# Optimization experiments

Hardware: AMD Instinct MI355X
Metric: run time of the kernel (lower is better)

Reference implementation:

```python
import jax, jax.numpy as jnp
import numpy as np

L, B, E, H, G = 4, 8, 1024, 16, 4096
N_IMG, T_TXT, V = 256, 64, 16385
EPS = 1e-6

def _ln(x, b, s=None):
    m = jnp.mean(x, axis=-1, keepdims=True)
    v = jnp.var(x, axis=-1, keepdims=True)
    y = (x - m) * jax.lax.rsqrt(v + EPS)
    if s is not None:
        y = y * s
    return y + b

def _attend(keys, values, queries, mask, w_out):
    # keys/values: [B,Tk,E]; queries: [B,Tq,E]; mask: [B,Tk]
    Bq, Tq, Eq = queries.shape
    d = Eq // H
    k = keys.reshape(keys.shape[0], -1, H, d)
    v = values.reshape(values.shape[0], -1, H, d)
    q = queries.reshape(Bq, Tq, H, d) / jnp.asarray(np.sqrt(d), queries.dtype)
    bias = jnp.where(mask, 0.0, -jnp.inf)
    w = jnp.einsum('bqhd,bkhd->bhqk', q, k) + bias[:, None, None, :]
    w = jax.nn.softmax(w, axis=-1)
    o = jnp.einsum('bhqk,bkhd->bqhd', w, v).reshape(Bq, Tq, Eq)
    return o @ w_out

def setup_inputs() -> dict:
    key = jax.random.key(0)
    ks = jax.random.split(key, 24)
    sc = 0.02
    nrm = lambda i, shape: sc * jax.random.normal(ks[i], shape, jnp.float32)
    return {
        "encoder_state": jax.random.normal(ks[0], (B, T_TXT, E), jnp.float32),
        "attention_state": 0.5 * jax.random.normal(ks[1], (L, 2 * B, N_IMG, E), jnp.float32),
        "attention_mask": jnp.ones((B, T_TXT), jnp.bool_),
        "prev_token": 16384,
        "token_index": 100,
        "embed_tok": nrm(2, (V, E)),
        "embed_pos": nrm(3, (N_IMG, E)),
        "lnemb_s": jnp.ones((E,), jnp.float32),
        "lnemb_b": jnp.zeros((E,), jnp.float32),
        "pre_self_ln_b": jnp.zeros((L, E), jnp.float32),
        "self_q": nrm(4, (L, E, E)),
        "self_k": nrm(5, (L, E, E)),
        "self_v": nrm(6, (L, E, E)),
        "self_o": nrm(7, (L, E, E)),
        "self_ln_s": jnp.ones((L, E), jnp.float32),
        "self_ln_b": jnp.zeros((L, E), jnp.float32),
        "pre_enc_ln_b": jnp.zeros((L, E), jnp.float32),
        "enc_q": nrm(8, (L, E, E)),
        "enc_k": nrm(9, (L, E, E)),
        "enc_v": nrm(10, (L, E, E)),
        "enc_o": nrm(11, (L, E, E)),
        "enc_ln_s": jnp.ones((L, E), jnp.float32),
        "enc_ln_b": jnp.zeros((L, E), jnp.float32),
        "glu_ln0_b": jnp.zeros((L, E), jnp.float32),
        "glu_fc0": nrm(12, (L, E, G)),
        "glu_fc1": nrm(13, (L, E, G)),
        "glu_ln1_b": jnp.zeros((L, G), jnp.float32),
        "glu_fc2": nrm(14, (L, G, E)),
        "final_ln_b": jnp.zeros((E,), jnp.float32),
        "lm_head_w": nrm(15, (E, V)),
    }

def reference(encoder_state, attention_state, attention_mask, prev_token, token_index, embed_tok, embed_pos, lnemb_s, lnemb_b, pre_self_ln_b, self_q, self_k, self_v, self_o, self_ln_s, self_ln_b, pre_enc_ln_b, enc_q, enc_k, enc_v, enc_o, enc_ln_s, enc_ln_b, glu_ln0_b, glu_fc0, glu_fc1, glu_ln1_b, glu_fc2, final_ln_b, lm_head_w):
    ones = jnp.ones((B, 1), jnp.int32)
    x = embed_tok[prev_token * ones] + embed_pos[token_index * ones]  # [B,1,E]
    x = _ln(x, lnemb_b, lnemb_s)
    self_mask = jnp.tile(jnp.arange(N_IMG) < token_index + 1, (B, 1))  # [B,N_IMG]

    def step(x, xs):
        (psb, sq, sk, sv, so, sls, slb, peb, eq, ek, ev, eo, els, elb,
         g0b, gf0, gf1, g1b, gf2, ast) = xs
        res = x
        h = _ln(x, psb)
        k, v, q = h @ sk, h @ sv, h @ sq
        ast = jax.lax.dynamic_update_slice(ast, jnp.concatenate([k, v]).astype(jnp.float32), (0, token_index, 0))
        h = _attend(ast[:B], ast[B:], q, self_mask, so).astype(x.dtype)
        x = res + _ln(h, slb, sls)
        res = x
        h = _ln(x, peb)
        h = _attend(encoder_state @ ek, encoder_state @ ev, h @ eq, attention_mask, eo)
        x = res + _ln(h, elb, els)
        res = x
        h = _ln(x, g0b)
        h = _ln(jax.nn.gelu(h @ gf0, approximate=False) * (h @ gf1), g1b)
        x = res + h @ gf2
        return x, ast

    xs = (pre_self_ln_b, self_q, self_k, self_v, self_o, self_ln_s, self_ln_b,
          pre_enc_ln_b, enc_q, enc_k, enc_v, enc_o, enc_ln_s, enc_ln_b,
          glu_ln0_b, glu_fc0, glu_fc1, glu_ln1_b, glu_fc2, attention_state)
    x, attention_state = jax.lax.scan(step, x, xs)
    x = _ln(x, final_ln_b)
    logits = x @ lm_head_w  # [B,1,V]
    return logits, attention_state
```

## Files before the change

### kernel.cpp

```cpp
#include <hip/hip_runtime.h>
#include <math.h>

#define EPSF 1e-6f

#define NL 4
#define NB 8
#define NE 1024
#define NH 16
#define NG 4096
#define NIMG 256
#define NTT 64
#define NV 16385
#define NVPAD 17408

#define P_QKV   0
#define P_FC01  786432
#define P_FC2   1835008
#define P_LM    2359296
#define SSPART  4587520
#define SEPART  4718592
#define XBUF    4849664
#define DH1     4857856
#define DX2     4866048
#define DX3     4874240
#define DH3     4882432
#define DHG     4890624
#define DHF     4923392
#define MFLAG   4931584

__device__ inline void wave_red2(float& a, float& b) {
#pragma unroll
  for (int o = 32; o; o >>= 1) { a += __shfl_xor(a, o); b += __shfl_xor(b, o); }
}

__device__ inline void block_red2(float& s, float& ss, float* tmp) {
  wave_red2(s, ss);
  int wv = threadIdx.x >> 6, ln = threadIdx.x & 63;
  if (ln == 0) { tmp[wv] = s; tmp[4 + wv] = ss; }
  __syncthreads();
  s = tmp[0] + tmp[1] + tmp[2] + tmp[3];
  ss = tmp[4] + tmp[5] + tmp[6] + tmp[7];
  __syncthreads();
}

__device__ inline float4 f4add(float4 a, float4 b) {
  return make_float4(a.x + b.x, a.y + b.y, a.z + b.z, a.w + b.w);
}

struct MvPartP {
  const float* W0; const float* W1; const float* W2;
  float* pout;
  const float* hsrc;
  int K, N, NPAD, CB, KS;
};

__global__ __launch_bounds__(256) void mv_part(MvPartP p) {
  __shared__ float h[8 * 64];
  const int tid = threadIdx.x;
  const int per = p.CB * p.KS;
  const int m = blockIdx.x / per, rem = blockIdx.x % per;
  const int ks = rem / p.CB, cb = rem % p.CB;
  const int BK = p.K / p.KS;
  const int k0 = ks * BK;
  const int n0 = cb * 1024;
  const int bk4 = BK >> 2;
  for (int i = tid; i < 8 * bk4; i += 256) {
    int r = i / bk4, q = i - r * bk4;
    reinterpret_cast<float4*>(h)[i] =
        *reinterpret_cast<const float4*>(p.hsrc + (size_t)r * p.K + k0 + q * 4);
  }
  __syncthreads();

  const int nb = n0 + tid * 4;
  if (nb >= p.N) return;
  const float* W = (m == 0) ? p.W0 : (m == 1) ? p.W1 : p.W2;
  float* pr = p.pout + (size_t)(m * p.KS + ks) * 8 * p.NPAD;
  const float* wp = W + (size_t)k0 * p.N + nb;

  if (nb + 3 < p.N) {
    float4 acc[8];
#pragma unroll
    for (int r = 0; r < 8; ++r) acc[r] = make_float4(0.f, 0.f, 0.f, 0.f);
    for (int kk = 0; kk < BK; kk += 8) {
      float4 w[8];
#pragma unroll
      for (int j = 0; j < 8; ++j)
        w[j] = *reinterpret_cast<const float4*>(wp + (size_t)(kk + j) * p.N);
#pragma unroll
      for (int j = 0; j < 8; ++j) {
#pragma unroll
        for (int r = 0; r < 8; ++r) {
          float hv = h[r * BK + kk + j];
          acc[r].x += hv * w[j].x; acc[r].y += hv * w[j].y;
          acc[r].z += hv * w[j].z; acc[r].w += hv * w[j].w;
        }
      }
    }
#pragma unroll
    for (int r = 0; r < 8; ++r)
      *reinterpret_cast<float4*>(pr + (size_t)r * p.NPAD + nb) = acc[r];
  } else {
    for (int c = 0; c < 4; ++c) {
      if (nb + c >= p.N) break;
      float acc[8] = {0.f, 0.f, 0.f, 0.f, 0.f, 0.f, 0.f, 0.f};
      for (int kk = 0; kk < BK; ++kk) {
        float w = wp[(size_t)kk * p.N + c];
#pragma unroll
        for (int r = 0; r < 8; ++r) acc[r] += h[r * BK + kk] * w;
      }
#pragma unroll
      for (int r = 0; r < 8; ++r) pr[(size_t)r * p.NPAD + nb + c] = acc[r];
    }
  }
}

__global__ __launch_bounds__(256) void embed_copy(const float* __restrict__ tok,
    const float* __restrict__ pos, const int* __restrict__ prev, const int* __restrict__ tixp,
    const float* __restrict__ lnb, const float* __restrict__ lns,
    const float* __restrict__ psb0, const void* __restrict__ maskp,
    float* __restrict__ x0, float* __restrict__ h1, unsigned* __restrict__ mflag,
    const float4* __restrict__ astv, float4* __restrict__ oastv) {
  __shared__ float tmp[8];
  int bid = blockIdx.x, tid = threadIdx.x;
  if (bid < 8) {
    int b = bid;
    const float* te = tok + (size_t)prev[0] * NE;
    const float* pe = pos + (size_t)tixp[0] * NE;
    float4 t4 = *reinterpret_cast<const float4*>(te + tid * 4);
    float4 p4 = *reinterpret_cast<const float4*>(pe + tid * 4);
    float4 v = make_float4(t4.x + p4.x, t4.y + p4.y, t4.z + p4.z, t4.w + p4.w);
    float s = v.x + v.y + v.z + v.w;
    float ss = v.x * v.x + v.y * v.y + v.z * v.z + v.w * v.w;
    block_red2(s, ss, tmp);
    float m = s / NE, rs = rsqrtf(ss / NE - m * m + EPSF);
    float4 sc = *reinterpret_cast<const float4*>(lns + tid * 4);
    float4 bi = *reinterpret_cast<const float4*>(lnb + tid * 4);
    float4 x;
    x.x = (v.x - m) * rs * sc.x + bi.x; x.y = (v.y - m) * rs * sc.y + bi.y;
    x.z = (v.z - m) * rs * sc.z + bi.z; x.w = (v.w - m) * rs * sc.w + bi.w;
    *reinterpret_cast<float4*>(x0 + (size_t)b * NE + tid * 4) = x;
    float s2 = x.x + x.y + x.z + x.w;
    float ss2 = x.x * x.x + x.y * x.y + x.z * x.z + x.w * x.w;
    block_red2(s2, ss2, tmp);
    float m2 = s2 / NE, rs2 = rsqrtf(ss2 / NE - m2 * m2 + EPSF);
    float4 b2 = *reinterpret_cast<const float4*>(psb0 + tid * 4);
    float4 o;
    o.x = (x.x - m2) * rs2 + b2.x; o.y = (x.y - m2) * rs2 + b2.y;
    o.z = (x.z - m2) * rs2 + b2.z; o.w = (x.w - m2) * rs2 + b2.w;
    *reinterpret_cast<float4*>(h1 + (size_t)b * NE + tid * 4) = o;
    return;
  }
  if (bid == 8) {
    __shared__ int f;
    if (tid == 0) f = 1;
    __syncthreads();
    if (tid < 128) { if (((const unsigned*)maskp)[tid] > 1u) f = 0; }
    __syncthreads();
    if (tid == 0) *mflag = f ? 1u : 2u;
  }
  const int n4 = NL * 16 * NIMG * (NE / 4);
  for (int i = (bid - 8) * 256 + tid; i < n4; i += 4096 * 256) oastv[i] = astv[i];
}

__global__ __launch_bounds__(256) void ln_fc2(const float* __restrict__ P,
    const float* __restrict__ resid, const float* __restrict__ bias,
    float* __restrict__ xout, float* __restrict__ hout, int KS) {
  __shared__ float tmp[8];
  int b = blockIdx.x, tid = threadIdx.x;
  int col = tid * 4;
  float4 acc = *reinterpret_cast<const float4*>(resid + (size_t)b * NE + col);
  const float* base = P + (size_t)b * 1024 + col;
  for (int ks = 0; ks < KS; ks += 8) {
    float4 w[8];
#pragma unroll
    for (int j = 0; j < 8; ++j)
      w[j] = *reinterpret_cast<const float4*>(base + (size_t)(ks + j) * 8192);
#pragma unroll
    for (int j = 0; j < 8; ++j) acc = f4add(acc, w[j]);
  }
  *reinterpret_cast<float4*>(xout + (size_t)b * NE + col) = acc;
  float s = acc.x + acc.y + acc.z + acc.w;
  float ss = acc.x * acc.x + acc.y * acc.y + acc.z * acc.z + acc.w * acc.w;
  block_red2(s, ss, tmp);
  float m = s / NE, rs = rsqrtf(ss / NE - m * m + EPSF);
  float4 bi = *reinterpret_cast<const float4*>(bias + col);
  float4 o;
  o.x = (acc.x - m) * rs + bi.x; o.y = (acc.y - m) * rs + bi.y;
  o.z = (acc.z - m) * rs + bi.z; o.w = (acc.w - m) * rs + bi.w;
  *reinterpret_cast<float4*>(hout + (size_t)b * NE + col) = o;
}

__global__ __launch_bounds__(256) void ln_res_sum(const float* __restrict__ xres,
    const float* __restrict__ part, const float* __restrict__ lns1,
    const float* __restrict__ lnb1, const float* __restrict__ lnb2,
    float* __restrict__ xstore, float* __restrict__ hout) {
  __shared__ float tmp[8];
  int b = blockIdx.x, tid = threadIdx.x;
  int col = tid * 4;
  float4 sv = make_float4(0.f, 0.f, 0.f, 0.f);
  const float* base = part + (size_t)b * 1024 + col;
#pragma unroll
  for (int h = 0; h < 16; h += 8) {
    float4 w[8];
#pragma unroll
    for (int j = 0; j < 8; ++j)
      w[j] = *reinterpret_cast<const float4*>(base + (size_t)(h + j) * 8192);
#pragma unroll
    for (int j = 0; j < 8; ++j) sv = f4add(sv, w[j]);
  }
  float s = sv.x + sv.y + sv.z + sv.w;
  float ss = sv.x * sv.x + sv.y * sv.y + sv.z * sv.z + sv.w * sv.w;
  block_red2(s, ss, tmp);
  float m1 = s / NE, rs1 = rsqrtf(ss / NE - m1 * m1 + EPSF);
  float4 xv = *reinterpret_cast<const float4*>(xres + (size_t)b * NE + col);
  float4 sc1 = *reinterpret_cast<const float4*>(lns1 + col);
  float4 b1 = *reinterpret_cast<const float4*>(lnb1 + col);
  float4 v;
  v.x = xv.x + (sv.x - m1) * rs1 * sc1.x + b1.x;
  v.y = xv.y + (sv.y - m1) * rs1 * sc1.y + b1.y;
  v.z = xv.z + (sv.z - m1) * rs1 * sc1.z + b1.z;
  v.w = xv.w + (sv.w - m1) * rs1 * sc1.w + b1.w;
  *reinterpret_cast<float4*>(xstore + (size_t)b * NE + col) = v;
  float s2 = v.x + v.y + v.z + v.w;
  float ss2 = v.x * v.x + v.y * v.y + v.z * v.z + v.w * v.w;
  block_red2(s2, ss2, tmp);
  float m2 = s2 / NE, rs2 = rsqrtf(ss2 / NE - m2 * m2 + EPSF);
  float4 b2 = *reinterpret_cast<const float4*>(lnb2 + col);
  float4 o;
  o.x = (v.x - m2) * rs2 + b2.x; o.y = (v.y - m2) * rs2 + b2.y;
  o.z = (v.z - m2) * rs2 + b2.z; o.w = (v.w - m2) * rs2 + b2.w;
  *reinterpret_cast<float4*>(hout + (size_t)b * NE + col) = o;
}

__global__ __launch_bounds__(256) void gelu_ln_sum(const float* __restrict__ P,
    const float* __restrict__ lnb, float* __restrict__ hout) {
  __shared__ float tmp[8];
  int b = blockIdx.x, tid = threadIdx.x;
  float4 g[4];
  float s = 0.f, ss = 0.f;
#pragma unroll
  for (int q = 0; q < 4; ++q) {
    int col = (tid + 256 * q) * 4;
    float4 a = make_float4(0.f, 0.f, 0.f, 0.f);
    float4 bb = make_float4(0.f, 0.f, 0.f, 0.f);
    const float* baseA = P + (size_t)b * 4096 + col;
    const float* baseB = P + ((size_t)16 * 8 + b) * 4096 + col;
#pragma unroll
    for (int ks = 0; ks < 16; ++ks) {
      a = f4add(a, *reinterpret_cast<const float4*>(baseA + (size_t)ks * 32768));
      bb = f4add(bb, *reinterpret_cast<const float4*>(baseB + (size_t)ks * 32768));
    }
    float4 gg;
    gg.x = 0.5f * a.x * (1.f + erff(a.x * 0.70710678118f)) * bb.x;
    gg.y = 0.5f * a.y * (1.f + erff(a.y * 0.70710678118f)) * bb.y;
    gg.z = 0.5f * a.z * (1.f + erff(a.z * 0.70710678118f)) * bb.z;
    gg.w = 0.5f * a.w * (1.f + erff(a.w * 0.70710678118f)) * bb.w;
    g[q] = gg;
    s += gg.x + gg.y + gg.z + gg.w;
    ss += gg.x * gg.x + gg.y * gg.y + gg.z * gg.z + gg.w * gg.w;
  }
  block_red2(s, ss, tmp);
  float m = s / NG, rs = rsqrtf(ss / NG - m * m + EPSF);
#pragma unroll
  for (int q = 0; q < 4; ++q) {
    int col = (tid + 256 * q) * 4;
    float4 bi = *reinterpret_cast<const float4*>(lnb + col);
    float4 o;
    o.x = (g[q].x - m) * rs + bi.x; o.y = (g[q].y - m) * rs + bi.y;
    o.z = (g[q].z - m) * rs + bi.z; o.w = (g[q].w - m) * rs + bi.w;
    *reinterpret_cast<float4*>(hout + (size_t)b * NG + col) = o;
  }
}

__global__ __launch_bounds__(256) void attn_fused(const float* __restrict__ Pqkv,
    const float* __restrict__ ast_l, const int* __restrict__ tixp,
    const float* __restrict__ Wso, float* __restrict__ spart, float* __restrict__ oast_l) {
  int b = blockIdx.x >> 4, hh = blockIdx.x & 15;
  int tid = threadIdx.x;
  int tix0 = tixp[0];
  int tixc = tix0 < 0 ? 0 : (tix0 > 255 ? 255 : tix0);
  int T = tixc + 1;
  __shared__ float qv[64];
  __shared__ float kf[64];
  __shared__ float vf[64];
  __shared__ float scb[256];
  __shared__ float red[256];
  __shared__ float pv[1024];
  __shared__ float ov[64];
  if (tid < 192) {
    int m = tid >> 6, d = tid & 63;
    const float* bp = Pqkv + (size_t)(m * 32) * 8192 + (size_t)b * 1024 + hh * 64 + d;
    float acc = 0.f;
#pragma unroll
    for (int ks = 0; ks < 32; ++ks) acc += bp[(size_t)ks * 8192];
    if (m == 2) qv[d] = acc * 0.125f;
    else {
      if (m == 0) kf[d] = acc; else vf[d] = acc;
      if (tix0 >= 0 && tix0 < NIMG) {
        int row = (m == 0) ? b : 8 + b;
        oast_l[((size_t)row * NIMG + tix0) * NE + hh * 64 + d] = acc;
      }
    }
  }
  __syncthreads();
  float sj = -INFINITY;
  if (tid < T) {
    const float* kr = (tid == tixc) ? kf : (ast_l + ((size_t)b * NIMG + tid) * NE + hh * 64);
    float s = 0.f;
#pragma unroll
    for (int d0 = 0; d0 < 64; d0 += 4) {
      float4 k4 = *reinterpret_cast<const float4*>(kr + d0);
      s += qv[d0] * k4.x + qv[d0 + 1] * k4.y + qv[d0 + 2] * k4.z + qv[d0 + 3] * k4.w;
    }
    sj = s;
  }
  red[tid] = sj; __syncthreads();
  for (int o = 128; o; o >>= 1) { if (tid < o) red[tid] = fmaxf(red[tid], red[tid + o]); __syncthreads(); }
  float mx = red[0]; __syncthreads();
  float e = (tid < T) ? __expf(sj - mx) : 0.f;
  red[tid] = e; __syncthreads();
  for (int o = 128; o; o >>= 1) { if (tid < o) red[tid] += red[tid + o]; __syncthreads(); }
  float inv = 1.f / red[0];
  scb[tid] = e * inv;
  __syncthreads();
  {
    int c = tid >> 4, d4 = (tid & 15) * 4;
    float4 a = make_float4(0.f, 0.f, 0.f, 0.f);
    for (int j = c; j < T; j += 16) {
      const float* vr = (j == tixc) ? vf : (ast_l + ((size_t)(8 + b) * NIMG + j) * NE + hh * 64);
      float4 v4 = *reinterpret_cast<const float4*>(vr + d4);
      float w = scb[j];
      a.x += w * v4.x; a.y += w * v4.y; a.z += w * v4.z; a.w += w * v4.w;
    }
    pv[c * 64 + d4 + 0] = a.x; pv[c * 64 + d4 + 1] = a.y;
    pv[c * 64 + d4 + 2] = a.z; pv[c * 64 + d4 + 3] = a.w;
  }
  __syncthreads();
  if (tid < 64) {
    float s = 0.f;
#pragma unroll
    for (int c = 0; c < 16; ++c) s += pv[c * 64 + tid];
    ov[tid] = s;
  }
  __syncthreads();
  {
    int nb = tid * 4;
    const float* wp = Wso + (size_t)(hh * 64) * NE + nb;
    float4 acc = make_float4(0.f, 0.f, 0.f, 0.f);
    for (int d = 0; d < 64; d += 8) {
      float4 w[8];
#pragma unroll
      for (int j = 0; j < 8; ++j)
        w[j] = *reinterpret_cast<const float4*>(wp + (size_t)(d + j) * NE);
#pragma unroll
      for (int j = 0; j < 8; ++j) {
        float o = ov[d + j];
        acc.x += o * w[j].x; acc.y += o * w[j].y; acc.z += o * w[j].z; acc.w += o * w[j].w;
      }
    }
    *reinterpret_cast<float4*>(spart + ((size_t)hh * 8 + b) * 1024 + nb) = acc;
  }
}

__global__ __launch_bounds__(256) void cross_fused(const float* __restrict__ xres,
    const float* __restrict__ sspart, const float* __restrict__ sls,
    const float* __restrict__ slb, const float* __restrict__ peb,
    const float* __restrict__ Weq, const float* __restrict__ Wek,
    const float* __restrict__ Wev, const float* __restrict__ Weo,
    const float* __restrict__ X, const void* __restrict__ maskp,
    const unsigned* __restrict__ mflag, float* __restrict__ x2store,
    float* __restrict__ spart) {
  int b = blockIdx.x >> 4, hh = blockIdx.x & 15;
  int tid = threadIdx.x;
  __shared__ float vecA[NE];
  __shared__ float vecB[NE];
  __shared__ float red[256];
  __shared__ float w_[NTT];
  __shared__ float qv[64];
  __shared__ float oe[64];
  __shared__ float tmp[8];
  int mi32 = (*mflag == 1u);
  {
    int col = tid * 4;
    float4 sv = make_float4(0.f, 0.f, 0.f, 0.f);
    const float* base = sspart + (size_t)b * 1024 + col;
#pragma unroll
    for (int h = 0; h < 16; h += 8) {
      float4 w[8];
#pragma unroll
      for (int j = 0; j < 8; ++j)
        w[j] = *reinterpret_cast<const float4*>(base + (size_t)(h + j) * 8192);
#pragma unroll
      for (int j = 0; j < 8; ++j) sv = f4add(sv, w[j]);
    }
    float s = sv.x + sv.y + sv.z + sv.w;
    float ss = sv.x * sv.x + sv.y * sv.y + sv.z * sv.z + sv.w * sv.w;
    block_red2(s, ss, tmp);
    float m1 = s / NE, rs1 = rsqrtf(ss / NE - m1 * m1 + EPSF);
    float4 xv = *reinterpret_cast<const float4*>(xres + (size_t)b * NE + col);
    float4 sc1 = *reinterpret_cast<const float4*>(sls + col);
    float4 b1 = *reinterpret_cast<const float4*>(slb + col);
    float4 v;
    v.x = xv.x + (sv.x - m1) * rs1 * sc1.x + b1.x;
    v.y = xv.y + (sv.y - m1) * rs1 * sc1.y + b1.y;
    v.z = xv.z + (sv.z - m1) * rs1 * sc1.z + b1.z;
    v.w = xv.w + (sv.w - m1) * rs1 * sc1.w + b1.w;
    if (hh == 0)
      *reinterpret_cast<float4*>(x2store + (size_t)b * NE + col) = v;
    float s2 = v.x + v.y + v.z + v.w;
    float ss2 = v.x * v.x + v.y * v.y + v.z * v.z + v.w * v.w;
    block_red2(s2, ss2, tmp);
    float m2 = s2 / NE, rs2 = rsqrtf(ss2 / NE - m2 * m2 + EPSF);
    float4 b2 = *reinterpret_cast<const float4*>(peb + col);
    float4 o;
    o.x = (v.x - m2) * rs2 + b2.x; o.y = (v.y - m2) * rs2 + b2.y;
    o.z = (v.z - m2) * rs2 + b2.z; o.w = (v.w - m2) * rs2 + b2.w;
    reinterpret_cast<float4*>(vecA)[tid] = o;
  }
  __syncthreads();

  {
    int d4 = (tid & 15) * 4, ech = tid >> 4;
    const float* base = Weq + hh * 64 + d4;
    float4 a = make_float4(0.f, 0.f, 0.f, 0.f);
    for (int e = ech * 64; e < ech * 64 + 64; e += 8) {
      float4 w[8];
#pragma unroll
      for (int j = 0; j < 8; ++j)
        w[j] = *reinterpret_cast<const float4*>(base + (size_t)(e + j) * NE);
#pragma unroll
      for (int j = 0; j < 8; ++j) {
        float hv = vecA[e + j];
        a.x += hv * w[j].x; a.y += hv * w[j].y; a.z += hv * w[j].z; a.w += hv * w[j].w;
      }
    }
    vecB[ech * 64 + d4 + 0] = a.x; vecB[ech * 64 + d4 + 1] = a.y;
    vecB[ech * 64 + d4 + 2] = a.z; vecB[ech * 64 + d4 + 3] = a.w;
  }
  __syncthreads();
  if (tid < 64) {
    float s = 0.f;
#pragma unroll
    for (int c = 0; c < 16; ++c) s += vecB[c * 64 + tid];
    qv[tid] = s;
  }
  __syncthreads();

  {
    float qwtmp[4];
#pragma unroll
    for (int jj = 0; jj < 4; ++jj) {
      int e = tid + 256 * jj;
      const float* wr = Wek + (size_t)e * NE + hh * 64;
      float a = 0.f;
#pragma unroll
      for (int d0 = 0; d0 < 64; d0 += 4) {
        float4 w4 = *reinterpret_cast<const float4*>(wr + d0);
        a += qv[d0] * w4.x + qv[d0 + 1] * w4.y + qv[d0 + 2] * w4.z + qv[d0 + 3] * w4.w;
      }
      qwtmp[jj] = a;
    }
#pragma unroll
    for (int jj = 0; jj < 4; ++jj) vecB[tid + 256 * jj] = qwtmp[jj];
  }
  __syncthreads();

  {
    int t = tid & 63, ec = tid >> 6;
    const float* xr = X + ((size_t)b * NTT + t) * NE + ec * 256;
    float part = 0.f;
#pragma unroll 4
    for (int i = 0; i < 256; i += 4) {
      float4 x4 = *reinterpret_cast<const float4*>(xr + i);
      part += vecB[ec * 256 + i] * x4.x + vecB[ec * 256 + i + 1] * x4.y +
              vecB[ec * 256 + i + 2] * x4.z + vecB[ec * 256 + i + 3] * x4.w;
    }
    red[ec * 64 + t] = part;
  }
  __syncthreads();
  float sco = -INFINITY;
  if (tid < 64) {
    float s = (red[tid] + red[64 + tid] + red[128 + tid] + red[192 + tid]) * 0.125f;
    int idx = b * NTT + tid;
    bool valid = mi32 ? (((const int*)maskp)[idx] != 0)
                      : (((const unsigned char*)maskp)[idx] != 0);
    sco = valid ? s : -INFINITY;
  }
  __syncthreads();
  red[tid] = (tid < 64) ? sco : -INFINITY; __syncthreads();
  for (int o = 128; o; o >>= 1) { if (tid < o) red[tid] = fmaxf(red[tid], red[tid + o]); __syncthreads(); }
  float mx = red[0]; __syncthreads();
  float e = (tid < 64) ? __expf(sco - mx) : 0.f;
  red[tid] = e; __syncthreads();
  for (int o = 128; o; o >>= 1) { if (tid < o) red[tid] += red[tid + o]; __syncthreads(); }
  if (tid < 64) w_[tid] = e / red[0];
  __syncthreads();

  {
    float4 a = make_float4(0.f, 0.f, 0.f, 0.f);
    const float* xb = X + (size_t)b * NTT * NE + tid * 4;
    for (int t = 0; t < NTT; t += 4) {
#pragma unroll
      for (int j = 0; j < 4; ++j) {
        float4 x4 = *reinterpret_cast<const float4*>(xb + (size_t)(t + j) * NE);
        float w = w_[t + j];
        a.x += w * x4.x; a.y += w * x4.y; a.z += w * x4.z; a.w += w * x4.w;
      }
    }
    reinterpret_cast<float4*>(vecA)[tid] = a;
  }
  __syncthreads();

  {
    int d4 = (tid & 15) * 4, ech = tid >> 4;
    const float* base = Wev + hh * 64 + d4;
    float4 a = make_float4(0.f, 0.f, 0.f, 0.f);
    for (int e = ech * 64; e < ech * 64 + 64; e += 8) {
      float4 w[8];
#pragma unroll
      for (int j = 0; j < 8; ++j)
        w[j] = *reinterpret_cast<const float4*>(base + (size_t)(e + j) * NE);
#pragma unroll
      for (int j = 0; j < 8; ++j) {
        float hv = vecA[e + j];
        a.x += hv * w[j].x; a.y += hv * w[j].y; a.z += hv * w[j].z; a.w += hv * w[j].w;
      }
    }
    vecB[ech * 64 + d4 + 0] = a.x; vecB[ech * 64 + d4 + 1] = a.y;
    vecB[ech * 64 + d4 + 2] = a.z; vecB[ech * 64 + d4 + 3] = a.w;
  }
  __syncthreads();
  if (tid < 64) {
    float s = 0.f;
#pragma unroll
    for (int c = 0; c < 16; ++c) s += vecB[c * 64 + tid];
    oe[tid] = s;
  }
  __syncthreads();

  {
    int nb = tid * 4;
    const float* wp = Weo + (size_t)(hh * 64) * NE + nb;
    float4 acc = make_float4(0.f, 0.f, 0.f, 0.f);
    for (int d = 0; d < 64; d += 8) {
      float4 w[8];
#pragma unroll
      for (int j = 0; j < 8; ++j)
        w[j] = *reinterpret_cast<const float4*>(wp + (size_t)(d + j) * NE);
#pragma unroll
      for (int j = 0; j < 8; ++j) {
        float o = oe[d + j];
        acc.x += o * w[j].x; acc.y += o * w[j].y; acc.z += o * w[j].z; acc.w += o * w[j].w;
      }
    }
    *reinterpret_cast<float4*>(spart + ((size_t)hh * 8 + b) * 1024 + nb) = acc;
  }
}

__global__ __launch_bounds__(256) void reduce_logits(const float* __restrict__ P,
                                                     float* __restrict__ logits) {
  int r = blockIdx.x / 17, cc = blockIdx.x % 17;
  int col = cc * 1024 + threadIdx.x * 4;
  if (col >= NV) return;
  if (col + 3 < NV) {
    const float* base = P + (size_t)r * NVPAD + col;
    float4 acc = make_float4(0.f, 0.f, 0.f, 0.f);
    for (int ks = 0; ks < 16; ks += 8) {
      float4 w[8];
#pragma unroll
      for (int j = 0; j < 8; ++j)
        w[j] = *reinterpret_cast<const float4*>(base + (size_t)(ks + j) * 8 * NVPAD);
#pragma unroll
      for (int j = 0; j < 8; ++j) acc = f4add(acc, w[j]);
    }
    *reinterpret_cast<float4*>(logits + (size_t)r * NV + col) = acc;
  } else {
    for (int c = 0; c < 4 && col + c < NV; ++c) {
      float a = 0.f;
      for (int ks = 0; ks < 16; ++ks) a += P[((size_t)ks * 8 + r) * NVPAD + col + c];
      logits[(size_t)r * NV + col + c] = a;
    }
  }
}

extern "C" void kernel_launch(void* const* d_in, const int* in_sizes, int n_in,
                              void* d_out, int out_size, void* d_ws, size_t ws_size,
                              hipStream_t stream) {
  const float* enc_state = (const float*)d_in[0];
  const float* ast_in    = (const float*)d_in[1];
  const void* amask      = d_in[2];
  const int* prev = (const int*)d_in[3];
  const int* tix  = (const int*)d_in[4];
  const float* embed_tok = (const float*)d_in[5];
  const float* embed_pos = (const float*)d_in[6];
  const float* lnemb_s = (const float*)d_in[7];
  const float* lnemb_b = (const float*)d_in[8];
  const float* psb = (const float*)d_in[9];
  const float* Wsq = (const float*)d_in[10];
  const float* Wsk = (const float*)d_in[11];
  const float* Wsv = (const float*)d_in[12];
  const float* Wso = (const float*)d_in[13];
  const float* sls = (const float*)d_in[14];
  const float* slb = (const float*)d_in[15];
  const float* peb = (const float*)d_in[16];
  const float* Weq = (const float*)d_in[17];
  const float* Wek = (const float*)d_in[18];
  const float* Wev = (const float*)d_in[19];
  const float* Weo = (const float*)d_in[20];
  const float* els = (const float*)d_in[21];
  const float* elb = (const float*)d_in[22];
  const float* g0b = (const float*)d_in[23];
  const float* Wf0 = (const float*)d_in[24];
  const float* Wf1 = (const float*)d_in[25];
  const float* g1b = (const float*)d_in[26];
  const float* Wf2 = (const float*)d_in[27];
  const float* flb = (const float*)d_in[28];
  const float* Wlm = (const float*)d_in[29];

  float* ws = (float*)d_ws;
  float* logits = (float*)d_out;
  float* out_ast = logits + (size_t)NB * NV;

  embed_copy<<<4104, 256, 0, stream>>>(embed_tok, embed_pos, prev, tix, lnemb_b, lnemb_s,
                                       psb, amask, ws + XBUF, ws + DH1,
                                       (unsigned*)(ws + MFLAG),
                                       (const float4*)ast_in, (float4*)out_ast);

  for (int l = 0; l < NL; ++l) {
    size_t wE = (size_t)l * NE * NE;
    size_t wG = (size_t)l * NE * NG;

    if (l > 0) {
      ln_fc2<<<NB, 256, 0, stream>>>(ws + P_FC2, ws + DX3, psb + (size_t)l * NE,
                                     ws + XBUF, ws + DH1, 64);
    }
    {
      MvPartP p{}; p.W0 = Wsk + wE; p.W1 = Wsv + wE; p.W2 = Wsq + wE;
      p.pout = ws + P_QKV; p.hsrc = ws + DH1;
      p.K = NE; p.N = NE; p.NPAD = NE; p.CB = 1; p.KS = 32;
      mv_part<<<3 * 32, 256, 0, stream>>>(p);
    }
    attn_fused<<<NB * NH, 256, 0, stream>>>(ws + P_QKV,
                                            ast_in + (size_t)l * 16 * NIMG * NE, tix,
                                            Wso + wE, ws + SSPART,
                                            out_ast + (size_t)l * 16 * NIMG * NE);
    cross_fused<<<NB * NH, 256, 0, stream>>>(ws + XBUF, ws + SSPART,
                                             sls + (size_t)l * NE, slb + (size_t)l * NE,
                                             peb + (size_t)l * NE,
                                             Weq + wE, Wek + wE, Wev + wE, Weo + wE,
                                             enc_state, amask,
                                             (const unsigned*)(ws + MFLAG),
                                             ws + DX2, ws + SEPART);
    ln_res_sum<<<NB, 256, 0, stream>>>(ws + DX2, ws + SEPART, els + (size_t)l * NE,
                                       elb + (size_t)l * NE, g0b + (size_t)l * NE,
                                       ws + DX3, ws + DH3);
    {
      MvPartP p{}; p.W0 = Wf0 + wG; p.W1 = Wf1 + wG;
      p.pout = ws + P_FC01; p.hsrc = ws + DH3;
      p.K = NE; p.N = NG; p.NPAD = NG; p.CB = 4; p.KS = 16;
      mv_part<<<2 * 4 * 16, 256, 0, stream>>>(p);
    }
    gelu_ln_sum<<<NB, 256, 0, stream>>>(ws + P_FC01, g1b + (size_t)l * NG, ws + DHG);
    {
      MvPartP p{}; p.W0 = Wf2 + (size_t)l * NG * NE;
      p.pout = ws + P_FC2; p.hsrc = ws + DHG;
      p.K = NG; p.N = NE; p.NPAD = NE; p.CB = 1; p.KS = 64;
      mv_part<<<64, 256, 0, stream>>>(p);
    }
  }
  ln_fc2<<<NB, 256, 0, stream>>>(ws + P_FC2, ws + DX3, flb, ws + XBUF, ws + DHF, 64);
  {
    MvPartP p{}; p.W0 = Wlm;
    p.pout = ws + P_LM; p.hsrc = ws + DHF;
    p.K = NE; p.N = NV; p.NPAD = NVPAD; p.CB = 17; p.KS = 16;
    mv_part<<<17 * 16, 256, 0, stream>>>(p);
  }
  reduce_logits<<<NB * 17, 256, 0, stream>>>(ws + P_LM, logits);
}
```

Before: 570.5 us.

## Fuse LayerNorm into matvec input staging and rebalance split-K partitioning

Partial sums of the residual and GELU outputs are now reduced by wider-grid combine kernels that also emit per-chunk mean/variance statistics. The following matvec kernel applies the LayerNorm while staging its input into shared memory, which removes the separate 8-block ln_fc2 and gelu_ln_sum kernels. The QKV, FC0/1 and FC2 matvecs also switch to a one-column-per-thread variant with more column blocks and fewer K splits, which shrinks the partial buffers and spreads the reduction work across more blocks. In exchange, every block recomputes the statistics, and scalar weight loads replace float4 loads.

```diff
diff --git a/kernel.cpp b/kernel.cpp
--- a/kernel.cpp
+++ b/kernel.cpp
@@ -14,19 +14,19 @@
 #define NVPAD 17408
 
 #define P_QKV   0
-#define P_FC01  786432
-#define P_FC2   1835008
-#define P_LM    2359296
-#define SSPART  4587520
-#define SEPART  4718592
-#define XBUF    4849664
-#define DH1     4857856
-#define DX2     4866048
-#define DX3     4874240
-#define DH3     4882432
-#define DHG     4890624
-#define DHF     4923392
-#define MFLAG   4931584
+#define P_FC01  393216
+#define P_FC2   917504
+#define P_LM    1179648
+#define SSPART  3407872
+#define SEPART  3538944
+#define XBUF    3670016
+#define DX2     3678208
+#define DX3     3686400
+#define DH3     3694592
+#define DG      3702784
+#define XSTAT   3735552
+#define GSTAT   3735616
+#define MFLAG   3735744
 
 __device__ inline void wave_red2(float& a, float& b) {
 #pragma unroll
@@ -47,79 +47,172 @@
   return make_float4(a.x + b.x, a.y + b.y, a.z + b.z, a.w + b.w);
 }
 
-struct MvPartP {
+struct MvP {
   const float* W0; const float* W1; const float* W2;
   float* pout;
   const float* hsrc;
-  int K, N, NPAD, CB, KS;
+  const float* xsrc;
+  const float* stats;
+  const float* bias;
+  int K, N, NPAD, CB, KS, mode, nchunk;
 };
 
-__global__ __launch_bounds__(256) void mv_part(MvPartP p) {
-  __shared__ float h[8 * 64];
+template <int C>
+__global__ __launch_bounds__(256) void mv_k(MvP p) {
+  __shared__ float h[8 * 128];
+  __shared__ float mrs[8][2];
   const int tid = threadIdx.x;
   const int per = p.CB * p.KS;
   const int m = blockIdx.x / per, rem = blockIdx.x % per;
   const int ks = rem / p.CB, cb = rem % p.CB;
   const int BK = p.K / p.KS;
   const int k0 = ks * BK;
-  const int n0 = cb * 1024;
+  const int n0 = cb * 256 * C;
   const int bk4 = BK >> 2;
-  for (int i = tid; i < 8 * bk4; i += 256) {
-    int r = i / bk4, q = i - r * bk4;
-    reinterpret_cast<float4*>(h)[i] =
-        *reinterpret_cast<const float4*>(p.hsrc + (size_t)r * p.K + k0 + q * 4);
-  }
-  __syncthreads();
-
-  const int nb = n0 + tid * 4;
-  if (nb >= p.N) return;
+
+  if (p.mode == 1) {
+    if (tid < 8) {
+      float s = 0.f, ss = 0.f;
+      for (int c = 0; c < p.nchunk; ++c) {
+        s += p.stats[(tid * p.nchunk + c) * 2];
+        ss += p.stats[(tid * p.nchunk + c) * 2 + 1];
+      }
+      float mean = s / p.K;
+      mrs[tid][0] = mean;
+      mrs[tid][1] = rsqrtf(ss / p.K - mean * mean + EPSF);
+    }
+    __syncthreads();
+    for (int i = tid; i < 8 * bk4; i += 256) {
+      int r = i / bk4, q = i - r * bk4;
+      float4 xv = *reinterpret_cast<const float4*>(p.xsrc + (size_t)r * p.K + k0 + q * 4);
+      float4 bi = *reinterpret_cast<const float4*>(p.bias + k0 + q * 4);
+      float mm = mrs[r][0], rs = mrs[r][1];
+      float4 o = make_float4((xv.x - mm) * rs + bi.x, (xv.y - mm) * rs + bi.y,
+                             (xv.z - mm) * rs + bi.z, (xv.w - mm) * rs + bi.w);
+      *reinterpret_cast<float4*>(h + r * BK + q * 4) = o;
+    }
+  } else {
+    for (int i = tid; i < 8 * bk4; i += 256) {
+      int r = i / bk4, q = i - r * bk4;
+      *reinterpret_cast<float4*>(h + r * BK + q * 4) =
+          *reinterpret_cast<const float4*>(p.hsrc + (size_t)r * p.K + k0 + q * 4);
+    }
+  }
+  __syncthreads();
+
   const float* W = (m == 0) ? p.W0 : (m == 1) ? p.W1 : p.W2;
   float* pr = p.pout + (size_t)(m * p.KS + ks) * 8 * p.NPAD;
-  const float* wp = W + (size_t)k0 * p.N + nb;
-
-  if (nb + 3 < p.N) {
-    float4 acc[8];
-#pragma unroll
-    for (int r = 0; r < 8; ++r) acc[r] = make_float4(0.f, 0.f, 0.f, 0.f);
+
+  if (C == 1) {
+    int col = n0 + tid;
+    if (col >= p.N) return;
+    const float* wp = W + (size_t)k0 * p.N + col;
+    float acc[8] = {0.f, 0.f, 0.f, 0.f, 0.f, 0.f, 0.f, 0.f};
     for (int kk = 0; kk < BK; kk += 8) {
-      float4 w[8];
-#pragma unroll
-      for (int j = 0; j < 8; ++j)
-        w[j] = *reinterpret_cast<const float4*>(wp + (size_t)(kk + j) * p.N);
+      float w[8];
+#pragma unroll
+      for (int j = 0; j < 8; ++j) w[j] = wp[(size_t)(kk + j) * p.N];
 #pragma unroll
       for (int j = 0; j < 8; ++j) {
 #pragma unroll
-        for (int r = 0; r < 8; ++r) {
-          float hv = h[r * BK + kk + j];
-          acc[r].x += hv * w[j].x; acc[r].y += hv * w[j].y;
-          acc[r].z += hv * w[j].z; acc[r].w += hv * w[j].w;
+        for (int r = 0; r < 8; ++r) acc[r] += h[r * BK + kk + j] * w[j];
+      }
+    }
+#pragma unroll
+    for (int r = 0; r < 8; ++r) pr[(size_t)r * p.NPAD + col] = acc[r];
+  } else {
+    int nb = n0 + tid * 4;
+    if (nb >= p.N) return;
+    const float* wp = W + (size_t)k0 * p.N + nb;
+    if (nb + 3 < p.N) {
+      float4 acc[8];
+#pragma unroll
+      for (int r = 0; r < 8; ++r) acc[r] = make_float4(0.f, 0.f, 0.f, 0.f);
+      for (int kk = 0; kk < BK; kk += 8) {
+        float4 w[8];
+#pragma unroll
+        for (int j = 0; j < 8; ++j)
+          w[j] = *reinterpret_cast<const float4*>(wp + (size_t)(kk + j) * p.N);
+#pragma unroll
+        for (int j = 0; j < 8; ++j) {
+#pragma unroll
+          for (int r = 0; r < 8; ++r) {
+            float hv = h[r * BK + kk + j];
+            acc[r].x += hv * w[j].x; acc[r].y += hv * w[j].y;
+            acc[r].z += hv * w[j].z; acc[r].w += hv * w[j].w;
+          }
         }
       }
-    }
-#pragma unroll
-    for (int r = 0; r < 8; ++r)
-      *reinterpret_cast<float4*>(pr + (size_t)r * p.NPAD + nb) = acc[r];
-  } else {
-    for (int c = 0; c < 4; ++c) {
-      if (nb + c >= p.N) break;
-      float acc[8] = {0.f, 0.f, 0.f, 0.f, 0.f, 0.f, 0.f, 0.f};
-      for (int kk = 0; kk < BK; ++kk) {
-        float w = wp[(size_t)kk * p.N + c];
-#pragma unroll
-        for (int r = 0; r < 8; ++r) acc[r] += h[r * BK + kk] * w;
-      }
-#pragma unroll
-      for (int r = 0; r < 8; ++r) pr[(size_t)r * p.NPAD + nb + c] = acc[r];
-    }
+#pragma unroll
+      for (int r = 0; r < 8; ++r)
+        *reinterpret_cast<float4*>(pr + (size_t)r * p.NPAD + nb) = acc[r];
+    } else {
+      for (int c = 0; c < 4; ++c) {
+        if (nb + c >= p.N) break;
+        float acc[8] = {0.f, 0.f, 0.f, 0.f, 0.f, 0.f, 0.f, 0.f};
+        for (int kk = 0; kk < BK; ++kk) {
+          float w = wp[(size_t)kk * p.N + c];
+#pragma unroll
+          for (int r = 0; r < 8; ++r) acc[r] += h[r * BK + kk] * w;
+        }
+#pragma unroll
+        for (int r = 0; r < 8; ++r) pr[(size_t)r * p.NPAD + nb + c] = acc[r];
+      }
+    }
+  }
+}
+
+__global__ __launch_bounds__(256) void combine_g(const float* __restrict__ P,
+    float* __restrict__ g, float* __restrict__ gstats) {
+  __shared__ float tmp[8];
+  int b = blockIdx.x >> 3, ch = blockIdx.x & 7;
+  int tid = threadIdx.x;
+  int col = ch * 512 + tid * 2;
+  const float* baseA = P + (size_t)b * NG + col;
+  const float* baseB = P + ((size_t)8 * 8 + b) * NG + col;
+  float2 a = make_float2(0.f, 0.f), bb = make_float2(0.f, 0.f);
+#pragma unroll
+  for (int ks = 0; ks < 8; ++ks) {
+    float2 pa = *reinterpret_cast<const float2*>(baseA + (size_t)ks * 8 * NG);
+    float2 pb = *reinterpret_cast<const float2*>(baseB + (size_t)ks * 8 * NG);
+    a.x += pa.x; a.y += pa.y; bb.x += pb.x; bb.y += pb.y;
+  }
+  float2 gg;
+  gg.x = 0.5f * a.x * (1.f + erff(a.x * 0.70710678118f)) * bb.x;
+  gg.y = 0.5f * a.y * (1.f + erff(a.y * 0.70710678118f)) * bb.y;
+  *reinterpret_cast<float2*>(g + (size_t)b * NG + col) = gg;
+  float s = gg.x + gg.y, ss = gg.x * gg.x + gg.y * gg.y;
+  block_red2(s, ss, tmp);
+  if (tid == 0) {
+    gstats[(b * 8 + ch) * 2] = s;
+    gstats[(b * 8 + ch) * 2 + 1] = ss;
+  }
+}
+
+__global__ __launch_bounds__(256) void combine_x(const float* __restrict__ P,
+    const float* __restrict__ resid, float* __restrict__ xout, float* __restrict__ xstats) {
+  __shared__ float tmp[8];
+  int b = blockIdx.x >> 2, ch = blockIdx.x & 3;
+  int tid = threadIdx.x;
+  int col = ch * 256 + tid;
+  float acc = resid[(size_t)b * NE + col];
+  const float* base = P + (size_t)b * NE + col;
+#pragma unroll
+  for (int ks = 0; ks < 32; ++ks) acc += base[(size_t)ks * 8 * NE];
+  xout[(size_t)b * NE + col] = acc;
+  float s = acc, ss = acc * acc;
+  block_red2(s, ss, tmp);
+  if (tid == 0) {
+    xstats[(b * 4 + ch) * 2] = s;
+    xstats[(b * 4 + ch) * 2 + 1] = ss;
   }
 }
 
 __global__ __launch_bounds__(256) void embed_copy(const float* __restrict__ tok,
     const float* __restrict__ pos, const int* __restrict__ prev, const int* __restrict__ tixp,
     const float* __restrict__ lnb, const float* __restrict__ lns,
-    const float* __restrict__ psb0, const void* __restrict__ maskp,
-    float* __restrict__ x0, float* __restrict__ h1, unsigned* __restrict__ mflag,
-    const float4* __restrict__ astv, float4* __restrict__ oastv) {
+    const void* __restrict__ maskp, float* __restrict__ x0, float* __restrict__ xstats,
+    unsigned* __restrict__ mflag, const float4* __restrict__ astv, float4* __restrict__ oastv) {
   __shared__ float tmp[8];
   int bid = blockIdx.x, tid = threadIdx.x;
   if (bid < 8) {
@@ -142,12 +235,11 @@
     float s2 = x.x + x.y + x.z + x.w;
     float ss2 = x.x * x.x + x.y * x.y + x.z * x.z + x.w * x.w;
     block_red2(s2, ss2, tmp);
-    float m2 = s2 / NE, rs2 = rsqrtf(ss2 / NE - m2 * m2 + EPSF);
-    float4 b2 = *reinterpret_cast<const float4*>(psb0 + tid * 4);
-    float4 o;
-    o.x = (x.x - m2) * rs2 + b2.x; o.y = (x.y - m2) * rs2 + b2.y;
-    o.z = (x.z - m2) * rs2 + b2.z; o.w = (x.w - m2) * rs2 + b2.w;
-    *reinterpret_cast<float4*>(h1 + (size_t)b * NE + tid * 4) = o;
+    if (tid == 0) {
+      xstats[(b * 4 + 0) * 2] = s2; xstats[(b * 4 + 0) * 2 + 1] = ss2;
+#pragma unroll
+      for (int c = 1; c < 4; ++c) { xstats[(b * 4 + c) * 2] = 0.f; xstats[(b * 4 + c) * 2 + 1] = 0.f; }
+    }
     return;
   }
   if (bid == 8) {
@@ -160,34 +252,6 @@
   }
   const int n4 = NL * 16 * NIMG * (NE / 4);
   for (int i = (bid - 8) * 256 + tid; i < n4; i += 4096 * 256) oastv[i] = astv[i];
-}
-
-__global__ __launch_bounds__(256) void ln_fc2(const float* __restrict__ P,
-    const float* __restrict__ resid, const float* __restrict__ bias,
-    float* __restrict__ xout, float* __restrict__ hout, int KS) {
-  __shared__ float tmp[8];
-  int b = blockIdx.x, tid = threadIdx.x;
-  int col = tid * 4;
-  float4 acc = *reinterpret_cast<const float4*>(resid + (size_t)b * NE + col);
-  const float* base = P + (size_t)b * 1024 + col;
-  for (int ks = 0; ks < KS; ks += 8) {
-    float4 w[8];
-#pragma unroll
-    for (int j = 0; j < 8; ++j)
-      w[j] = *reinterpret_cast<const float4*>(base + (size_t)(ks + j) * 8192);
-#pragma unroll
-    for (int j = 0; j < 8; ++j) acc = f4add(acc, w[j]);
-  }
-  *reinterpret_cast<float4*>(xout + (size_t)b * NE + col) = acc;
-  float s = acc.x + acc.y + acc.z + acc.w;
-  float ss = acc.x * acc.x + acc.y * acc.y + acc.z * acc.z + acc.w * acc.w;
-  block_red2(s, ss, tmp);
-  float m = s / NE, rs = rsqrtf(ss / NE - m * m + EPSF);
-  float4 bi = *reinterpret_cast<const float4*>(bias + col);
-  float4 o;
-  o.x = (acc.x - m) * rs + bi.x; o.y = (acc.y - m) * rs + bi.y;
-  o.z = (acc.z - m) * rs + bi.z; o.w = (acc.w - m) * rs + bi.w;
-  *reinterpret_cast<float4*>(hout + (size_t)b * NE + col) = o;
 }
 
 __global__ __launch_bounds__(256) void ln_res_sum(const float* __restrict__ xres,
@@ -232,46 +296,6 @@
   *reinterpret_cast<float4*>(hout + (size_t)b * NE + col) = o;
 }
 
-__global__ __launch_bounds__(256) void gelu_ln_sum(const float* __restrict__ P,
-    const float* __restrict__ lnb, float* __restrict__ hout) {
-  __shared__ float tmp[8];
-  int b = blockIdx.x, tid = threadIdx.x;
-  float4 g[4];
-  float s = 0.f, ss = 0.f;
-#pragma unroll
-  for (int q = 0; q < 4; ++q) {
-    int col = (tid + 256 * q) * 4;
-    float4 a = make_float4(0.f, 0.f, 0.f, 0.f);
-    float4 bb = make_float4(0.f, 0.f, 0.f, 0.f);
-    const float* baseA = P + (size_t)b * 4096 + col;
-    const float* baseB = P + ((size_t)16 * 8 + b) * 4096 + col;
-#pragma unroll
-    for (int ks = 0; ks < 16; ++ks) {
-      a = f4add(a, *reinterpret_cast<const float4*>(baseA + (size_t)ks * 32768));
-      bb = f4add(bb, *reinterpret_cast<const float4*>(baseB + (size_t)ks * 32768));
-    }
-    float4 gg;
-    gg.x = 0.5f * a.x * (1.f + erff(a.x * 0.70710678118f)) * bb.x;
-    gg.y = 0.5f * a.y * (1.f + erff(a.y * 0.70710678118f)) * bb.y;
-    gg.z = 0.5f * a.z * (1.f + erff(a.z * 0.70710678118f)) * bb.z;
-    gg.w = 0.5f * a.w * (1.f + erff(a.w * 0.70710678118f)) * bb.w;
-    g[q] = gg;
-    s += gg.x + gg.y + gg.z + gg.w;
-    ss += gg.x * gg.x + gg.y * gg.y + gg.z * gg.z + gg.w * gg.w;
-  }
-  block_red2(s, ss, tmp);
-  float m = s / NG, rs = rsqrtf(ss / NG - m * m + EPSF);
-#pragma unroll
-  for (int q = 0; q < 4; ++q) {
-    int col = (tid + 256 * q) * 4;
-    float4 bi = *reinterpret_cast<const float4*>(lnb + col);
-    float4 o;
-    o.x = (g[q].x - m) * rs + bi.x; o.y = (g[q].y - m) * rs + bi.y;
-    o.z = (g[q].z - m) * rs + bi.z; o.w = (g[q].w - m) * rs + bi.w;
-    *reinterpret_cast<float4*>(hout + (size_t)b * NG + col) = o;
-  }
-}
-
 __global__ __launch_bounds__(256) void attn_fused(const float* __restrict__ Pqkv,
     const float* __restrict__ ast_l, const int* __restrict__ tixp,
     const float* __restrict__ Wso, float* __restrict__ spart, float* __restrict__ oast_l) {
@@ -289,10 +313,10 @@
   __shared__ float ov[64];
   if (tid < 192) {
     int m = tid >> 6, d = tid & 63;
-    const float* bp = Pqkv + (size_t)(m * 32) * 8192 + (size_t)b * 1024 + hh * 64 + d;
+    const float* bp = Pqkv + (size_t)(m * 16) * 8192 + (size_t)b * 1024 + hh * 64 + d;
     float acc = 0.f;
 #pragma unroll
-    for (int ks = 0; ks < 32; ++ks) acc += bp[(size_t)ks * 8192];
+    for (int ks = 0; ks < 16; ++ks) acc += bp[(size_t)ks * 8192];
     if (m == 2) qv[d] = acc * 0.125f;
     else {
       if (m == 0) kf[d] = acc; else vf[d] = acc;
@@ -622,7 +646,7 @@
   float* out_ast = logits + (size_t)NB * NV;
 
   embed_copy<<<4104, 256, 0, stream>>>(embed_tok, embed_pos, prev, tix, lnemb_b, lnemb_s,
-                                       psb, amask, ws + XBUF, ws + DH1,
+                                       amask, ws + XBUF, ws + XSTAT,
                                        (unsigned*)(ws + MFLAG),
                                        (const float4*)ast_in, (float4*)out_ast);
 
@@ -630,15 +654,12 @@
     size_t wE = (size_t)l * NE * NE;
     size_t wG = (size_t)l * NE * NG;
 
-    if (l > 0) {
-      ln_fc2<<<NB, 256, 0, stream>>>(ws + P_FC2, ws + DX3, psb + (size_t)l * NE,
-                                     ws + XBUF, ws + DH1, 64);
-    }
     {
-      MvPartP p{}; p.W0 = Wsk + wE; p.W1 = Wsv + wE; p.W2 = Wsq + wE;
-      p.pout = ws + P_QKV; p.hsrc = ws + DH1;
-      p.K = NE; p.N = NE; p.NPAD = NE; p.CB = 1; p.KS = 32;
-      mv_part<<<3 * 32, 256, 0, stream>>>(p);
+      MvP p{}; p.W0 = Wsk + wE; p.W1 = Wsv + wE; p.W2 = Wsq + wE;
+      p.pout = ws + P_QKV; p.xsrc = ws + XBUF; p.stats = ws + XSTAT;
+      p.bias = psb + (size_t)l * NE;
+      p.K = NE; p.N = NE; p.NPAD = NE; p.CB = 4; p.KS = 16; p.mode = 1; p.nchunk = 4;
+      mv_k<1><<<3 * 4 * 16, 256, 0, stream>>>(p);
     }
     attn_fused<<<NB * NH, 256, 0, stream>>>(ws + P_QKV,
                                             ast_in + (size_t)l * 16 * NIMG * NE, tix,
@@ -655,25 +676,26 @@
                                        elb + (size_t)l * NE, g0b + (size_t)l * NE,
                                        ws + DX3, ws + DH3);
     {
-      MvPartP p{}; p.W0 = Wf0 + wG; p.W1 = Wf1 + wG;
+      MvP p{}; p.W0 = Wf0 + wG; p.W1 = Wf1 + wG;
       p.pout = ws + P_FC01; p.hsrc = ws + DH3;
-      p.K = NE; p.N = NG; p.NPAD = NG; p.CB = 4; p.KS = 16;
-      mv_part<<<2 * 4 * 16, 256, 0, stream>>>(p);
-    }
-    gelu_ln_sum<<<NB, 256, 0, stream>>>(ws + P_FC01, g1b + (size_t)l * NG, ws + DHG);
+      p.K = NE; p.N = NG; p.NPAD = NG; p.CB = 16; p.KS = 8; p.mode = 0;
+      mv_k<1><<<2 * 16 * 8, 256, 0, stream>>>(p);
+    }
+    combine_g<<<64, 256, 0, stream>>>(ws + P_FC01, ws + DG, ws + GSTAT);
     {
-      MvPartP p{}; p.W0 = Wf2 + (size_t)l * NG * NE;
-      p.pout = ws + P_FC2; p.hsrc = ws + DHG;
-      p.K = NG; p.N = NE; p.NPAD = NE; p.CB = 1; p.KS = 64;
-      mv_part<<<64, 256, 0, stream>>>(p);
-    }
-  }
-  ln_fc2<<<NB, 256, 0, stream>>>(ws + P_FC2, ws + DX3, flb, ws + XBUF, ws + DHF, 64);
-  {
-    MvPartP p{}; p.W0 = Wlm;
-    p.pout = ws + P_LM; p.hsrc = ws + DHF;
-    p.K = NE; p.N = NV; p.NPAD = NVPAD; p.CB = 17; p.KS = 16;
-    mv_part<<<17 * 16, 256, 0, stream>>>(p);
+      MvP p{}; p.W0 = Wf2 + (size_t)l * NG * NE;
+      p.pout = ws + P_FC2; p.xsrc = ws + DG; p.stats = ws + GSTAT;
+      p.bias = g1b + (size_t)l * NG;
+      p.K = NG; p.N = NE; p.NPAD = NE; p.CB = 4; p.KS = 32; p.mode = 1; p.nchunk = 8;
+      mv_k<1><<<4 * 32, 256, 0, stream>>>(p);
+    }
+    combine_x<<<32, 256, 0, stream>>>(ws + P_FC2, ws + DX3, ws + XBUF, ws + XSTAT);
+  }
+  {
+    MvP p{}; p.W0 = Wlm;
+    p.pout = ws + P_LM; p.xsrc = ws + XBUF; p.stats = ws + XSTAT; p.bias = flb;
+    p.K = NE; p.N = NV; p.NPAD = NVPAD; p.CB = 17; p.KS = 16; p.mode = 1; p.nchunk = 4;
+    mv_k<4><<<17 * 16, 256, 0, stream>>>(p);
   }
   reduce_logits<<<NB * 17, 256, 0, stream>>>(ws + P_LM, logits);
 }
```

Result: faster. 479.6 us (median of 2 runs) (-15.9%).
